# Kernel tuning notes

Measured on AMD Instinct MI355X. Metric: run time of the kernel, lower is better.

The kernel has to match this reference:

```python
import jax, jax.numpy as jnp
import numpy as np
import math

D_MODEL = 512
N_HEAD = 8
D_FF = 2048
B, S, S_ENC = 2, 2048, 2048
EPS = 1e-5


def _linear_params(key, d_in, d_out):
    kw, kb = jax.random.split(key)
    w = jax.random.normal(kw, (d_in, d_out), dtype=jnp.float32) * 0.02
    b = jax.random.normal(kb, (d_out,), dtype=jnp.float32) * 0.02
    return w, b


def setup_inputs() -> dict:
    key = jax.random.key(0)
    ks = jax.random.split(key, 16)
    dec = jax.random.normal(ks[0], (B, S, D_MODEL), dtype=jnp.float32)
    enc = jax.random.normal(ks[1], (B, S_ENC, D_MODEL), dtype=jnp.float32)
    src_mask = jnp.ones((B, 1, 1, S_ENC), dtype=jnp.int32)  # no padding
    tgt_mask = jnp.tril(jnp.ones((S, S), dtype=jnp.int32))[None, None]  # causal
    inp = {"dec": dec, "enc": enc, "src_mask": src_mask, "tgt_mask": tgt_mask}
    # self-attention projections
    for i, nm in enumerate(["sa_wq", "sa_wk", "sa_wv", "sa_wo"]):
        w, b = _linear_params(ks[2 + i], D_MODEL, D_MODEL)
        inp[nm], inp[nm.replace("w", "b")] = w, b
    # cross-attention projections
    for i, nm in enumerate(["ca_wq", "ca_wk", "ca_wv", "ca_wo"]):
        w, b = _linear_params(ks[6 + i], D_MODEL, D_MODEL)
        inp[nm], inp[nm.replace("w", "b")] = w, b
    # FFN
    inp["ffn_w1"], inp["ffn_b1"] = _linear_params(ks[10], D_MODEL, D_FF)
    inp["ffn_w2"], inp["ffn_b2"] = _linear_params(ks[11], D_FF, D_MODEL)
    # LayerNorms (gamma=1, beta=0 init as in torch)
    for i in (1, 2, 3):
        inp[f"ln{i}_g"] = jnp.ones((D_MODEL,), dtype=jnp.float32)
        inp[f"ln{i}_b"] = jnp.zeros((D_MODEL,), dtype=jnp.float32)
    return inp


def _layer_norm(x, g, b):
    mu = jnp.mean(x, axis=-1, keepdims=True)
    var = jnp.mean(jnp.square(x - mu), axis=-1, keepdims=True)
    return (x - mu) * jax.lax.rsqrt(var + EPS) * g + b


def _mha(xq, xkv, wq, bq, wk, bk, wv, bv, wo, bo, mask):
    Bq, Sq, D = xq.shape
    Sk = xkv.shape[1]
    d_k = D // N_HEAD
    def split(x, s):
        return x.reshape(x.shape[0], s, N_HEAD, d_k).transpose(0, 2, 1, 3)  # [B,H,S,dk]
    q = split(xq @ wq + bq, Sq)
    k = split(xkv @ wk + bk, Sk)
    v = split(xkv @ wv + bv, Sk)
    scores = jnp.einsum("bhqd,bhkd->bhqk", q, k) / math.sqrt(d_k)
    if mask is not None:
        scores = jnp.where(mask == 0, jnp.float32(-1e9), scores)
    attn = jax.nn.softmax(scores, axis=-1)
    out = jnp.einsum("bhqk,bhkd->bhqd", attn, v)
    out = out.transpose(0, 2, 1, 3).reshape(Bq, Sq, D)
    return out @ wo + bo


def reference(dec, enc, src_mask, tgt_mask,
              sa_wq, sa_bq, sa_wk, sa_bk, sa_wv, sa_bv, sa_wo, sa_bo,
              ca_wq, ca_bq, ca_wk, ca_bk, ca_wv, ca_bv, ca_wo, ca_bo,
              ffn_w1, ffn_b1, ffn_w2, ffn_b2,
              ln1_g, ln1_b, ln2_g, ln2_b, ln3_g, ln3_b):
    # dropout is identity in eval mode
    x = _mha(dec, dec, sa_wq, sa_bq, sa_wk, sa_bk, sa_wv, sa_bv, sa_wo, sa_bo, tgt_mask)
    x = _layer_norm(x + dec, ln1_g, ln1_b)
    _x = x
    x = _mha(x, enc, ca_wq, ca_bq, ca_wk, ca_bk, ca_wv, ca_bv, ca_wo, ca_bo, src_mask)
    x = _layer_norm(x + _x, ln2_g, ln2_b)
    _x = x
    x = jax.nn.relu(x @ ffn_w1 + ffn_b1) @ ffn_w2 + ffn_b2
    x = _layer_norm(x + _x, ln3_g, ln3_b)
    return x
```

## Files before the change

### kernel.cpp

```cpp
#include <hip/hip_runtime.h>


#define D_MODEL 512
#define NHEAD 8
#define DK 64
#define SEQ 2048
#define MTOK 4096
#define DFF 2048

typedef __attribute__((ext_vector_type(8))) short bf16x8;
typedef __attribute__((ext_vector_type(4))) float f32x4;

__device__ __forceinline__ unsigned short f2bf(float x) {
  unsigned u = __float_as_uint(x);
  u += 0x7FFF + ((u >> 16) & 1);
  return (unsigned short)(u >> 16);
}
__device__ __forceinline__ unsigned pack2(float a, float b) {
  return (unsigned)f2bf(a) | ((unsigned)f2bf(b) << 16);
}
__device__ __forceinline__ void load_lds16(const unsigned short* g, unsigned short* l) {
  __builtin_amdgcn_global_load_lds(
      (const __attribute__((address_space(1))) void*)g,
      (__attribute__((address_space(3))) void*)l, 16, 0, 0);
}

struct WDesc { const float* src; unsigned short* dst; int K; int N; };
struct WPack { WDesc d[10]; };

__global__ __launch_bounds__(256)
void wprep_kernel(WPack p) {
  const WDesc wd = p.d[blockIdx.y];
  const int ntx = wd.N >> 5;
  const int ntile = (wd.K >> 5) * ntx;
  if ((int)blockIdx.x >= ntile) return;
  const int n0 = (blockIdx.x % ntx) * 32;
  const int k0 = (blockIdx.x / ntx) * 32;
  __shared__ float T[32][33];
  const int tid = threadIdx.x;
  {
    const int r = tid >> 3, c4 = (tid & 7) * 4;
    float4 v = *(const float4*)(wd.src + (long)(k0 + r) * wd.N + n0 + c4);
    T[r][c4] = v.x; T[r][c4 + 1] = v.y; T[r][c4 + 2] = v.z; T[r][c4 + 3] = v.w;
  }
  __syncthreads();
  {
    const int n = tid >> 3, kq = (tid & 7) * 4;
    ushort4 o;
    o.x = f2bf(T[kq + 0][n]); o.y = f2bf(T[kq + 1][n]);
    o.z = f2bf(T[kq + 2][n]); o.w = f2bf(T[kq + 3][n]);
    *(ushort4*)(wd.dst + (long)(n0 + n) * wd.K + k0 + kq) = o;
  }
}

__global__ __launch_bounds__(256)
void cast_kernel(const float* __restrict__ s, unsigned short* __restrict__ d, int n8) {
  const int i = blockIdx.x * 256 + threadIdx.x;
  if (i >= n8) return;
  float4 a = *(const float4*)(s + (long)i * 8);
  float4 b = *(const float4*)(s + (long)i * 8 + 4);
  uint4 o;
  o.x = pack2(a.x, a.y); o.y = pack2(a.z, a.w);
  o.z = pack2(b.x, b.y); o.w = pack2(b.z, b.w);
  *(uint4*)(d + (long)i * 8) = o;
}

template<int MODE, int BM>
__global__ __launch_bounds__(256)
void gemm_bf16(const unsigned short* __restrict__ A, const unsigned short* __restrict__ Wt,
               const float* __restrict__ b0, const float* __restrict__ b1,
               const float* __restrict__ b2, const float* res,
               const float* __restrict__ lnm, const float* __restrict__ lnr,
               const float* __restrict__ lng, const float* __restrict__ lnbt,
               unsigned short* __restrict__ o0, unsigned short* __restrict__ o1,
               unsigned short* __restrict__ o2, float* of,
               int M, int N, int K, float scale0) {
  constexpr int MF = BM / 32;
  __shared__ unsigned short As[BM * 32];
  __shared__ unsigned short Bs[2048];
  const int tid = threadIdx.x;
  const int w = tid >> 6, lane = tid & 63, g = lane >> 4, li = lane & 15;
  const int m0 = blockIdx.x * BM, n0 = blockIdx.y * 64;
  const int wm = w >> 1, wn = w & 1;

  f32x4 acc[MF][2] = {};
  const int bkg = tid >> 6, bn = tid & 63;
  const unsigned short* Bp = Wt + (long)(n0 + bn) * K + bkg * 8;

  const unsigned short* Ap0;
  const unsigned short* Ap1 = nullptr;
  if constexpr (BM == 128) {
    Ap0 = A + (long)(m0 + (tid & 127)) * K + (tid >> 7) * 8;
    Ap1 = A + (long)(m0 + (tid & 127)) * K + ((tid >> 7) + 2) * 8;
  } else {
    Ap0 = A + (long)(m0 + (tid & 63)) * K + (tid >> 6) * 8;
  }

  for (int k0 = 0; k0 < K; k0 += 32) {
    __syncthreads();
    load_lds16(Ap0 + k0, &As[(w * 64) * 8]);
    if constexpr (BM == 128) load_lds16(Ap1 + k0, &As[(256 + w * 64) * 8]);
    load_lds16(Bp + k0, &Bs[(w * 64) * 8]);
    __syncthreads();
    bf16x8 af[MF], bfr[2];
#pragma unroll
    for (int mf = 0; mf < MF; mf++)
      af[mf] = *(const bf16x8*)&As[(g * BM + wm * (BM / 2) + mf * 16 + li) * 8];
#pragma unroll
    for (int nf = 0; nf < 2; nf++)
      bfr[nf] = *(const bf16x8*)&Bs[(g * 64 + wn * 32 + nf * 16 + li) * 8];
#pragma unroll
    for (int mf = 0; mf < MF; mf++)
#pragma unroll
      for (int nf = 0; nf < 2; nf++)
        acc[mf][nf] = __builtin_amdgcn_mfma_f32_16x16x32_bf16(af[mf], bfr[nf], acc[mf][nf], 0, 0, 0);
  }

#pragma unroll
  for (int nf = 0; nf < 2; nf++) {
    const int c = n0 + wn * 32 + nf * 16 + li;
    float bias, scl = 1.f;
    unsigned short* hdst = nullptr;
    float lngv = 0.f, lnbv = 0.f;
    if constexpr (MODE == 0) {
      const int which = c >> 9;
      bias = (which == 0 ? b0 : (which == 1 ? b1 : b2))[c & 511];
      if (which == 0) scl = scale0;
      hdst = which == 0 ? o0 : (which == 1 ? o1 : o2);
    } else {
      bias = b0[c];
      if constexpr (MODE == 3) { lngv = lng[c]; lnbv = lnbt[c]; }
    }
#pragma unroll
    for (int mf = 0; mf < MF; mf++) {
#pragma unroll
      for (int j = 0; j < 4; j++) {
        const int r = m0 + wm * (BM / 2) + mf * 16 + g * 4 + j;
        float v = acc[mf][nf][j] + bias;
        if constexpr (MODE == 0) {
          v *= scl;
          const int b = r >> 11, s = r & (SEQ - 1), h = (c >> 6) & 7, d = c & 63;
          hdst[(((long)(b * NHEAD + h)) * SEQ + s) * DK + d] = f2bf(v);
        } else if constexpr (MODE == 1) {
          v += res[(long)r * N + c];
          of[(long)r * N + c] = v;
        } else if constexpr (MODE == 2) {
          o0[(long)r * N + c] = f2bf(fmaxf(v, 0.f));
        } else {
          const float xr = res[(long)r * N + c];
          v += (xr - lnm[r]) * lnr[r] * lngv + lnbv;
          of[(long)r * N + c] = v;
        }
      }
    }
  }
}

template<bool CAUSAL>
__global__ __launch_bounds__(256)
void attn_bf16(const unsigned short* __restrict__ Qg, const unsigned short* __restrict__ Kg,
               const unsigned short* __restrict__ Vg, float* __restrict__ Opart,
               float* __restrict__ Mst, float* __restrict__ Lst) {
  __shared__ unsigned short SM[16384];
  unsigned short* const Qp = SM;
  unsigned short* const Kp = SM + 8192;
  unsigned short* const Vt = SM + 12288;
  const int tid = threadIdx.x;
  const int w = tid >> 6, lane = tid & 63, g = lane >> 4, li = lane & 15;
  const int qb = blockIdx.x, bh = blockIdx.y, ck = blockIdx.z;
  const int q0 = qb * 128;
  const long base = (long)bh * SEQ * DK;
  unsigned short* const Pl = SM + w * 2048;

#pragma unroll
  for (int i = 0; i < 4; i++) {
    const int idx = i * 256 + tid;
    const int dg = idx >> 7, q = idx & 127;
    load_lds16(Qg + base + (long)(q0 + q) * DK + dg * 8, &Qp[(i * 256 + w * 64) * 8]);
  }
  __syncthreads();
  bf16x8 bq[2][2];
#pragma unroll
  for (int qf = 0; qf < 2; qf++)
#pragma unroll
    for (int ks = 0; ks < 2; ks++)
      bq[qf][ks] = *(const bf16x8*)&Qp[((ks * 4 + g) * 128 + w * 32 + qf * 16 + li) * 8];

  f32x4 oacc[2][4] = {};
  float mrun[2] = {-1e30f, -1e30f};
  float denom[2] = {0.f, 0.f};

  const int vdg = tid >> 5;
  const int vs0 = (tid & 31) * 2;
  const int vsg = vs0 >> 3, vso = vs0 & 7;

  const int tbeg = CAUSAL ? ck : ck * 8;
  const int tend = CAUSAL ? (2 * qb + 2) : (ck * 8 + 8);
  const int tstep = CAUSAL ? 4 : 1;
  for (int t = tbeg; t < tend; t += tstep) {
    const int k0 = t * 64;
    __syncthreads();
#pragma unroll
    for (int i = 0; i < 2; i++) {
      const int idx = i * 256 + tid;
      const int dg = idx >> 6, kk = idx & 63;
      load_lds16(Kg + base + (long)(k0 + kk) * DK + dg * 8, &Kp[(i * 256 + w * 64) * 8]);
    }
    {
      const unsigned short* vsrc = Vg + base + (long)(k0 + vs0) * DK + vdg * 8;
      uint4 r0 = *(const uint4*)vsrc;
      uint4 r1 = *(const uint4*)(vsrc + DK);
      unsigned short u0[8], u1[8];
      *(uint4*)u0 = r0; *(uint4*)u1 = r1;
#pragma unroll
      for (int e = 0; e < 8; e++) {
        const int d = vdg * 8 + e;
        const int dsw = d ^ (vsg & 7);
        *(unsigned*)&Vt[(vsg * 64 + dsw) * 8 + vso] =
            (unsigned)u0[e] | ((unsigned)u1[e] << 16);
      }
    }
    __syncthreads();

    f32x4 sacc[4][2] = {};
#pragma unroll
    for (int ks = 0; ks < 2; ks++) {
#pragma unroll
      for (int kf = 0; kf < 4; kf++) {
        bf16x8 ka = *(const bf16x8*)&Kp[((ks * 4 + g) * 64 + kf * 16 + li) * 8];
#pragma unroll
        for (int qf = 0; qf < 2; qf++)
          sacc[kf][qf] = __builtin_amdgcn_mfma_f32_16x16x32_bf16(ka, bq[qf][ks], sacc[kf][qf], 0, 0, 0);
      }
    }
    if (CAUSAL && t >= 2 * qb) {
#pragma unroll
      for (int kf = 0; kf < 4; kf++)
#pragma unroll
        for (int qf = 0; qf < 2; qf++)
#pragma unroll
          for (int j = 0; j < 4; j++) {
            const int kg_ = k0 + kf * 16 + g * 4 + j;
            const int qg_ = q0 + w * 32 + qf * 16 + li;
            if (kg_ > qg_) sacc[kf][qf][j] = -1e30f;
          }
    }
    float corrv[2];
#pragma unroll
    for (int qf = 0; qf < 2; qf++) {
      float mx = -1e30f;
#pragma unroll
      for (int kf = 0; kf < 4; kf++)
#pragma unroll
        for (int j = 0; j < 4; j++) mx = fmaxf(mx, sacc[kf][qf][j]);
      mx = fmaxf(mx, __shfl_xor(mx, 16, 64));
      mx = fmaxf(mx, __shfl_xor(mx, 32, 64));
      const float mn = fmaxf(mrun[qf], mx);
      const float corr = exp2f(mrun[qf] - mn);
      mrun[qf] = mn;
      float ps = 0.f;
#pragma unroll
      for (int kf = 0; kf < 4; kf++)
#pragma unroll
        for (int j = 0; j < 4; j++) {
          const float p = exp2f(sacc[kf][qf][j] - mn);
          sacc[kf][qf][j] = p;
          ps += p;
        }
      ps += __shfl_xor(ps, 16, 64);
      ps += __shfl_xor(ps, 32, 64);
      denom[qf] = denom[qf] * corr + ps;
      corrv[qf] = corr;
    }
#pragma unroll
    for (int mf = 0; mf < 2; mf++)
#pragma unroll
      for (int j = 0; j < 4; j++) {
        const float cf = __shfl(corrv[mf], g * 4 + j, 64);
#pragma unroll
        for (int df = 0; df < 4; df++) oacc[mf][df][j] *= cf;
      }
#pragma unroll
    for (int kf = 0; kf < 4; kf++)
#pragma unroll
      for (int qf = 0; qf < 2; qf++) {
        uint2 pv;
        pv.x = pack2(sacc[kf][qf][0], sacc[kf][qf][1]);
        pv.y = pack2(sacc[kf][qf][2], sacc[kf][qf][3]);
        *(uint2*)&Pl[((kf * 2 + (g >> 1)) * 32 + qf * 16 + li) * 8 + (g & 1) * 4] = pv;
      }
#pragma unroll
    for (int ks2 = 0; ks2 < 2; ks2++) {
      const int sg = ks2 * 4 + g;
#pragma unroll
      for (int mf = 0; mf < 2; mf++) {
        bf16x8 pa = *(const bf16x8*)&Pl[(sg * 32 + mf * 16 + li) * 8];
#pragma unroll
        for (int df = 0; df < 4; df++) {
          bf16x8 vb = *(const bf16x8*)&Vt[(sg * 64 + ((df * 16 + li) ^ (sg & 7))) * 8];
          oacc[mf][df] = __builtin_amdgcn_mfma_f32_16x16x32_bf16(pa, vb, oacc[mf][df], 0, 0, 0);
        }
      }
    }
  }

  const long pbase = (long)(ck * 16 + bh) * SEQ;
  if (g == 0) {
#pragma unroll
    for (int qf = 0; qf < 2; qf++) {
      const int q = q0 + w * 32 + qf * 16 + li;
      Mst[pbase + q] = mrun[qf];
      Lst[pbase + q] = denom[qf];
    }
  }
#pragma unroll
  for (int mf = 0; mf < 2; mf++)
#pragma unroll
    for (int j = 0; j < 4; j++) {
      const int q = q0 + w * 32 + mf * 16 + g * 4 + j;
      float* op = Opart + (pbase + q) * 64;
#pragma unroll
      for (int df = 0; df < 4; df++) op[df * 16 + li] = oacc[mf][df][j];
    }
}

__global__ __launch_bounds__(256)
void combine_kernel(const float* __restrict__ Opart, const float* __restrict__ Mst,
                    const float* __restrict__ Lst, unsigned short* __restrict__ AOb) {
  const int row = blockIdx.x * 4 + (threadIdx.x >> 6);
  const int lane = threadIdx.x & 63;
  const int bh = row >> 11, q = row & (SEQ - 1);
  float m[4], l[4], mstar = -1e30f;
#pragma unroll
  for (int c = 0; c < 4; c++) {
    m[c] = Mst[((long)c * 16 + bh) * SEQ + q];
    l[c] = Lst[((long)c * 16 + bh) * SEQ + q];
    mstar = fmaxf(mstar, m[c]);
  }
  float den = 0.f, o = 0.f;
#pragma unroll
  for (int c = 0; c < 4; c++) {
    const float wgt = exp2f(m[c] - mstar);
    den += wgt * l[c];
    o += wgt * Opart[(((long)c * 16 + bh) * SEQ + q) * 64 + lane];
  }
  const int b = bh >> 3, h = bh & 7;
  AOb[((long)(b * SEQ + q)) * D_MODEL + h * DK + lane] = f2bf(o / den);
}

template<int V>
__global__ __launch_bounds__(256)
void ln_kernel(const float* __restrict__ x, const float* __restrict__ gam,
               const float* __restrict__ bet, float* __restrict__ outf,
               unsigned short* __restrict__ outb, float* __restrict__ mu_s,
               float* __restrict__ rs_s) {
  const int row = blockIdx.x * 4 + (threadIdx.x >> 6);
  const int lane = threadIdx.x & 63;
  const float* xr = x + (long)row * D_MODEL;
  float4 v0 = *(const float4*)&xr[lane * 8];
  float4 v1 = *(const float4*)&xr[lane * 8 + 4];
  float xv[8] = {v0.x, v0.y, v0.z, v0.w, v1.x, v1.y, v1.z, v1.w};
  float s = 0.f, s2 = 0.f;
#pragma unroll
  for (int i = 0; i < 8; i++) { s += xv[i]; s2 = fmaf(xv[i], xv[i], s2); }
#pragma unroll
  for (int off = 32; off > 0; off >>= 1) {
    s += __shfl_xor(s, off, 64);
    s2 += __shfl_xor(s2, off, 64);
  }
  const float mu = s * (1.f / D_MODEL);
  const float var = fmaxf(s2 * (1.f / D_MODEL) - mu * mu, 0.f);
  const float rstd = rsqrtf(var + 1e-5f);
  float y[8];
#pragma unroll
  for (int i = 0; i < 8; i++) {
    const int c = lane * 8 + i;
    y[i] = (xv[i] - mu) * rstd * gam[c] + bet[c];
  }
  if constexpr (V == 0) {
    uint4 o;
    o.x = pack2(y[0], y[1]); o.y = pack2(y[2], y[3]);
    o.z = pack2(y[4], y[5]); o.w = pack2(y[6], y[7]);
    *(uint4*)(outb + (long)row * D_MODEL + lane * 8) = o;
    if (lane == 0) { mu_s[row] = mu; rs_s[row] = rstd; }
  } else {
    float* orow = outf + (long)row * D_MODEL + lane * 8;
    *(float4*)orow = make_float4(y[0], y[1], y[2], y[3]);
    *(float4*)(orow + 4) = make_float4(y[4], y[5], y[6], y[7]);
  }
}

extern "C" void kernel_launch(void* const* d_in, const int* in_sizes, int n_in,
                              void* d_out, int out_size, void* d_ws, size_t ws_size,
                              hipStream_t stream) {
  const float* dec = (const float*)d_in[0];
  const float* enc = (const float*)d_in[1];
  const float* sa_wq = (const float*)d_in[4];
  const float* sa_bq = (const float*)d_in[5];
  const float* sa_wk = (const float*)d_in[6];
  const float* sa_bk = (const float*)d_in[7];
  const float* sa_wv = (const float*)d_in[8];
  const float* sa_bv = (const float*)d_in[9];
  const float* sa_wo = (const float*)d_in[10];
  const float* sa_bo = (const float*)d_in[11];
  const float* ca_wq = (const float*)d_in[12];
  const float* ca_bq = (const float*)d_in[13];
  const float* ca_wk = (const float*)d_in[14];
  const float* ca_bk = (const float*)d_in[15];
  const float* ca_wv = (const float*)d_in[16];
  const float* ca_bv = (const float*)d_in[17];
  const float* ca_wo = (const float*)d_in[18];
  const float* ca_bo = (const float*)d_in[19];
  const float* ffn_w1 = (const float*)d_in[20];
  const float* ffn_b1 = (const float*)d_in[21];
  const float* ffn_w2 = (const float*)d_in[22];
  const float* ffn_b2 = (const float*)d_in[23];
  const float* ln1_g = (const float*)d_in[24];
  const float* ln1_b = (const float*)d_in[25];
  const float* ln2_g = (const float*)d_in[26];
  const float* ln2_b = (const float*)d_in[27];
  const float* ln3_g = (const float*)d_in[28];
  const float* ln3_b = (const float*)d_in[29];

  char* wsb = (char*)d_ws;
  unsigned short* dec_bf = (unsigned short*)wsb;
  float* Opart = (float*)wsb;
  float* Mst = (float*)(wsb + 33554432);
  float* Lst = (float*)(wsb + 34078720);
  unsigned short* MIDb = (unsigned short*)wsb;
  size_t off = 34603008;
  unsigned short* qkv_t = (unsigned short*)(wsb + off); off += 1572864;
  unsigned short* wo_t  = (unsigned short*)(wsb + off); off += 524288;
  unsigned short* cq_t  = (unsigned short*)(wsb + off); off += 524288;
  unsigned short* ckv_t = (unsigned short*)(wsb + off); off += 1048576;
  unsigned short* co_t  = (unsigned short*)(wsb + off); off += 524288;
  unsigned short* f1_t  = (unsigned short*)(wsb + off); off += 2097152;
  unsigned short* f2_t  = (unsigned short*)(wsb + off); off += 2097152;
  unsigned short* enc_bf = (unsigned short*)(wsb + off); off += 4194304;
  unsigned short* Qb  = (unsigned short*)(wsb + off); off += 4194304;
  unsigned short* Kb  = (unsigned short*)(wsb + off); off += 4194304;
  unsigned short* Vb  = (unsigned short*)(wsb + off); off += 4194304;
  unsigned short* AOb = (unsigned short*)(wsb + off); off += 4194304;
  unsigned short* X1b = (unsigned short*)(wsb + off); off += 4194304;
  unsigned short* X2b = (unsigned short*)(wsb + off); off += 4194304;
  float* R   = (float*)(wsb + off); off += 8388608;
  float* mu1 = (float*)(wsb + off); off += 16384;
  float* rs1 = (float*)(wsb + off); off += 16384;
  float* mu2 = (float*)(wsb + off); off += 16384;
  float* rs2 = (float*)(wsb + off); off += 16384;

  dim3 blk(256);
  const float QS = 0.125f * 1.44269504f;

  WPack wp;
  wp.d[0] = {sa_wq, qkv_t, 512, 512};
  wp.d[1] = {sa_wk, qkv_t + 262144, 512, 512};
  wp.d[2] = {sa_wv, qkv_t + 524288, 512, 512};
  wp.d[3] = {sa_wo, wo_t, 512, 512};
  wp.d[4] = {ca_wq, cq_t, 512, 512};
  wp.d[5] = {ca_wk, ckv_t, 512, 512};
  wp.d[6] = {ca_wv, ckv_t + 262144, 512, 512};
  wp.d[7] = {ca_wo, co_t, 512, 512};
  wp.d[8] = {ffn_w1, f1_t, 512, 2048};
  wp.d[9] = {ffn_w2, f2_t, 2048, 512};
  wprep_kernel<<<dim3(1024, 10), blk, 0, stream>>>(wp);
  cast_kernel<<<1024, blk, 0, stream>>>(dec, dec_bf, 262144);
  cast_kernel<<<1024, blk, 0, stream>>>(enc, enc_bf, 262144);

  gemm_bf16<0, 128><<<dim3(32, 24), blk, 0, stream>>>(dec_bf, qkv_t, sa_bq, sa_bk, sa_bv,
      nullptr, nullptr, nullptr, nullptr, nullptr, Qb, Kb, Vb, nullptr, MTOK, 1536, 512, QS);
  attn_bf16<true><<<dim3(16, 16, 4), blk, 0, stream>>>(Qb, Kb, Vb, Opart, Mst, Lst);
  combine_kernel<<<8192, blk, 0, stream>>>(Opart, Mst, Lst, AOb);
  gemm_bf16<1, 64><<<dim3(64, 8), blk, 0, stream>>>(AOb, wo_t, sa_bo, nullptr, nullptr,
      dec, nullptr, nullptr, nullptr, nullptr, nullptr, nullptr, nullptr, R, MTOK, 512, 512, 1.f);
  ln_kernel<0><<<1024, blk, 0, stream>>>(R, ln1_g, ln1_b, nullptr, X1b, mu1, rs1);

  gemm_bf16<0, 64><<<dim3(64, 8), blk, 0, stream>>>(X1b, cq_t, ca_bq, nullptr, nullptr,
      nullptr, nullptr, nullptr, nullptr, nullptr, Qb, nullptr, nullptr, nullptr, MTOK, 512, 512, QS);
  gemm_bf16<0, 128><<<dim3(32, 16), blk, 0, stream>>>(enc_bf, ckv_t, ca_bk, ca_bv, nullptr,
      nullptr, nullptr, nullptr, nullptr, nullptr, Kb, Vb, nullptr, nullptr, MTOK, 1024, 512, 1.f);
  attn_bf16<false><<<dim3(16, 16, 4), blk, 0, stream>>>(Qb, Kb, Vb, Opart, Mst, Lst);
  combine_kernel<<<8192, blk, 0, stream>>>(Opart, Mst, Lst, AOb);
  gemm_bf16<3, 64><<<dim3(64, 8), blk, 0, stream>>>(AOb, co_t, ca_bo, nullptr, nullptr,
      R, mu1, rs1, ln1_g, ln1_b, nullptr, nullptr, nullptr, R, MTOK, 512, 512, 1.f);
  ln_kernel<0><<<1024, blk, 0, stream>>>(R, ln2_g, ln2_b, nullptr, X2b, mu2, rs2);

  gemm_bf16<2, 128><<<dim3(32, 32), blk, 0, stream>>>(X2b, f1_t, ffn_b1, nullptr, nullptr,
      nullptr, nullptr, nullptr, nullptr, nullptr, MIDb, nullptr, nullptr, nullptr, MTOK, 2048, 512, 1.f);
  gemm_bf16<3, 64><<<dim3(64, 8), blk, 0, stream>>>(MIDb, f2_t, ffn_b2, nullptr, nullptr,
      R, mu2, rs2, ln2_g, ln2_b, nullptr, nullptr, nullptr, R, MTOK, 512, 2048, 1.f);
  ln_kernel<1><<<1024, blk, 0, stream>>>(R, ln3_g, ln3_b, (float*)d_out, nullptr, nullptr, nullptr);
}
```

Before: 435.0 us.

## Generalize GEMM tile width, add lazy softmax rescale and fast exp/bf16 pack

The GEMM kernel gains a BN template parameter so all launches use 128x128 or 128x64 tiles, which increases reuse per block and reduces the block count. The attention softmax now skips the running-max update and the output rescale unless some row's max grows by more than 8 (in log2 units), leaving the lazy rescaling decision uniform across the wave. exp2f is replaced with the hardware exp2 builtin, and bf16 packing uses the v_cvt_pk_bf16_f32 instruction. Larger tiles cut occupancy and leave fewer blocks for the 512x512 GEMMs, which can hurt load balance across the 256 CUs.

```diff
diff --git a/kernel.cpp b/kernel.cpp
--- a/kernel.cpp
+++ b/kernel.cpp
@@ -11,6 +11,12 @@
 typedef __attribute__((ext_vector_type(8))) short bf16x8;
 typedef __attribute__((ext_vector_type(4))) float f32x4;
 
+#if __has_builtin(__builtin_amdgcn_exp2f)
+#define EXP2(x) __builtin_amdgcn_exp2f(x)
+#else
+#define EXP2(x) exp2f(x)
+#endif
+
 __device__ __forceinline__ unsigned short f2bf(float x) {
   unsigned u = __float_as_uint(x);
   u += 0x7FFF + ((u >> 16) & 1);
@@ -18,6 +24,11 @@
 }
 __device__ __forceinline__ unsigned pack2(float a, float b) {
   return (unsigned)f2bf(a) | ((unsigned)f2bf(b) << 16);
+}
+__device__ __forceinline__ unsigned cvtpk(float lo, float hi) {
+  unsigned r;
+  asm("v_cvt_pk_bf16_f32 %0, %1, %2" : "=v"(r) : "v"(lo), "v"(hi));
+  return r;
 }
 __device__ __forceinline__ void load_lds16(const unsigned short* g, unsigned short* l) {
   __builtin_amdgcn_global_load_lds(
@@ -65,7 +76,7 @@
   *(uint4*)(d + (long)i * 8) = o;
 }
 
-template<int MODE, int BM>
+template<int MODE, int BM, int BN>
 __global__ __launch_bounds__(256)
 void gemm_bf16(const unsigned short* __restrict__ A, const unsigned short* __restrict__ Wt,
                const float* __restrict__ b0, const float* __restrict__ b1,
@@ -75,50 +86,53 @@
                unsigned short* __restrict__ o0, unsigned short* __restrict__ o1,
                unsigned short* __restrict__ o2, float* of,
                int M, int N, int K, float scale0) {
-  constexpr int MF = BM / 32;
+  constexpr int MF = BM / 32, NF = BN / 32;
+  constexpr int AI = BM / 64, BI = BN / 64;
   __shared__ unsigned short As[BM * 32];
-  __shared__ unsigned short Bs[2048];
+  __shared__ unsigned short Bs[BN * 32];
   const int tid = threadIdx.x;
   const int w = tid >> 6, lane = tid & 63, g = lane >> 4, li = lane & 15;
-  const int m0 = blockIdx.x * BM, n0 = blockIdx.y * 64;
+  const int m0 = blockIdx.x * BM, n0 = blockIdx.y * BN;
   const int wm = w >> 1, wn = w & 1;
 
-  f32x4 acc[MF][2] = {};
-  const int bkg = tid >> 6, bn = tid & 63;
-  const unsigned short* Bp = Wt + (long)(n0 + bn) * K + bkg * 8;
-
-  const unsigned short* Ap0;
-  const unsigned short* Ap1 = nullptr;
-  if constexpr (BM == 128) {
-    Ap0 = A + (long)(m0 + (tid & 127)) * K + (tid >> 7) * 8;
-    Ap1 = A + (long)(m0 + (tid & 127)) * K + ((tid >> 7) + 2) * 8;
-  } else {
-    Ap0 = A + (long)(m0 + (tid & 63)) * K + (tid >> 6) * 8;
+  f32x4 acc[MF][NF] = {};
+  const unsigned short* Ap[AI];
+  const unsigned short* Bp[BI];
+#pragma unroll
+  for (int i = 0; i < AI; i++) {
+    const int idx = i * 256 + tid;
+    Ap[i] = A + (long)(m0 + (idx % BM)) * K + (idx / BM) * 8;
+  }
+#pragma unroll
+  for (int i = 0; i < BI; i++) {
+    const int idx = i * 256 + tid;
+    Bp[i] = Wt + (long)(n0 + (idx % BN)) * K + (idx / BN) * 8;
   }
 
   for (int k0 = 0; k0 < K; k0 += 32) {
     __syncthreads();
-    load_lds16(Ap0 + k0, &As[(w * 64) * 8]);
-    if constexpr (BM == 128) load_lds16(Ap1 + k0, &As[(256 + w * 64) * 8]);
-    load_lds16(Bp + k0, &Bs[(w * 64) * 8]);
+#pragma unroll
+    for (int i = 0; i < AI; i++) load_lds16(Ap[i] + k0, &As[(i * 256 + w * 64) * 8]);
+#pragma unroll
+    for (int i = 0; i < BI; i++) load_lds16(Bp[i] + k0, &Bs[(i * 256 + w * 64) * 8]);
     __syncthreads();
-    bf16x8 af[MF], bfr[2];
+    bf16x8 af[MF], bfr[NF];
 #pragma unroll
     for (int mf = 0; mf < MF; mf++)
       af[mf] = *(const bf16x8*)&As[(g * BM + wm * (BM / 2) + mf * 16 + li) * 8];
 #pragma unroll
-    for (int nf = 0; nf < 2; nf++)
-      bfr[nf] = *(const bf16x8*)&Bs[(g * 64 + wn * 32 + nf * 16 + li) * 8];
+    for (int nf = 0; nf < NF; nf++)
+      bfr[nf] = *(const bf16x8*)&Bs[(g * BN + wn * (BN / 2) + nf * 16 + li) * 8];
 #pragma unroll
     for (int mf = 0; mf < MF; mf++)
 #pragma unroll
-      for (int nf = 0; nf < 2; nf++)
+      for (int nf = 0; nf < NF; nf++)
         acc[mf][nf] = __builtin_amdgcn_mfma_f32_16x16x32_bf16(af[mf], bfr[nf], acc[mf][nf], 0, 0, 0);
   }
 
 #pragma unroll
-  for (int nf = 0; nf < 2; nf++) {
-    const int c = n0 + wn * 32 + nf * 16 + li;
+  for (int nf = 0; nf < NF; nf++) {
+    const int c = n0 + wn * (BN / 2) + nf * 16 + li;
     float bias, scl = 1.f;
     unsigned short* hdst = nullptr;
     float lngv = 0.f, lnbv = 0.f;
@@ -245,48 +259,60 @@
             if (kg_ > qg_) sacc[kf][qf][j] = -1e30f;
           }
     }
-    float corrv[2];
+    float mx[2];
 #pragma unroll
     for (int qf = 0; qf < 2; qf++) {
-      float mx = -1e30f;
+      float a = fmaxf(fmaxf(sacc[0][qf][0], sacc[0][qf][1]), fmaxf(sacc[0][qf][2], sacc[0][qf][3]));
+      float b = fmaxf(fmaxf(sacc[1][qf][0], sacc[1][qf][1]), fmaxf(sacc[1][qf][2], sacc[1][qf][3]));
+      float c = fmaxf(fmaxf(sacc[2][qf][0], sacc[2][qf][1]), fmaxf(sacc[2][qf][2], sacc[2][qf][3]));
+      float d = fmaxf(fmaxf(sacc[3][qf][0], sacc[3][qf][1]), fmaxf(sacc[3][qf][2], sacc[3][qf][3]));
+      float m_ = fmaxf(fmaxf(a, b), fmaxf(c, d));
+      m_ = fmaxf(m_, __shfl_xor(m_, 16, 64));
+      m_ = fmaxf(m_, __shfl_xor(m_, 32, 64));
+      mx[qf] = m_;
+    }
+    const int full = !__all((mx[0] - mrun[0] <= 8.f) && (mx[1] - mrun[1] <= 8.f));
+    float corrv[2] = {1.f, 1.f};
+    if (full) {
+#pragma unroll
+      for (int qf = 0; qf < 2; qf++) {
+        const float mn = fmaxf(mrun[qf], mx[qf]);
+        corrv[qf] = EXP2(mrun[qf] - mn);
+        mrun[qf] = mn;
+      }
+    }
+#pragma unroll
+    for (int qf = 0; qf < 2; qf++) {
+      float ps = 0.f;
 #pragma unroll
       for (int kf = 0; kf < 4; kf++)
 #pragma unroll
-        for (int j = 0; j < 4; j++) mx = fmaxf(mx, sacc[kf][qf][j]);
-      mx = fmaxf(mx, __shfl_xor(mx, 16, 64));
-      mx = fmaxf(mx, __shfl_xor(mx, 32, 64));
-      const float mn = fmaxf(mrun[qf], mx);
-      const float corr = exp2f(mrun[qf] - mn);
-      mrun[qf] = mn;
-      float ps = 0.f;
-#pragma unroll
-      for (int kf = 0; kf < 4; kf++)
-#pragma unroll
         for (int j = 0; j < 4; j++) {
-          const float p = exp2f(sacc[kf][qf][j] - mn);
+          const float p = EXP2(sacc[kf][qf][j] - mrun[qf]);
           sacc[kf][qf][j] = p;
           ps += p;
         }
       ps += __shfl_xor(ps, 16, 64);
       ps += __shfl_xor(ps, 32, 64);
-      denom[qf] = denom[qf] * corr + ps;
-      corrv[qf] = corr;
-    }
-#pragma unroll
-    for (int mf = 0; mf < 2; mf++)
-#pragma unroll
-      for (int j = 0; j < 4; j++) {
-        const float cf = __shfl(corrv[mf], g * 4 + j, 64);
-#pragma unroll
-        for (int df = 0; df < 4; df++) oacc[mf][df][j] *= cf;
-      }
+      denom[qf] = denom[qf] * corrv[qf] + ps;
+    }
+    if (full) {
+#pragma unroll
+      for (int mf = 0; mf < 2; mf++)
+#pragma unroll
+        for (int j = 0; j < 4; j++) {
+          const float cf = __shfl(corrv[mf], g * 4 + j, 64);
+#pragma unroll
+          for (int df = 0; df < 4; df++) oacc[mf][df][j] *= cf;
+        }
+    }
 #pragma unroll
     for (int kf = 0; kf < 4; kf++)
 #pragma unroll
       for (int qf = 0; qf < 2; qf++) {
         uint2 pv;
-        pv.x = pack2(sacc[kf][qf][0], sacc[kf][qf][1]);
-        pv.y = pack2(sacc[kf][qf][2], sacc[kf][qf][3]);
+        pv.x = cvtpk(sacc[kf][qf][0], sacc[kf][qf][1]);
+        pv.y = cvtpk(sacc[kf][qf][2], sacc[kf][qf][3]);
         *(uint2*)&Pl[((kf * 2 + (g >> 1)) * 32 + qf * 16 + li) * 8 + (g & 1) * 4] = pv;
       }
 #pragma unroll
@@ -340,7 +366,7 @@
   float den = 0.f, o = 0.f;
 #pragma unroll
   for (int c = 0; c < 4; c++) {
-    const float wgt = exp2f(m[c] - mstar);
+    const float wgt = EXP2(m[c] - mstar);
     den += wgt * l[c];
     o += wgt * Opart[(((long)c * 16 + bh) * SEQ + q) * 64 + lane];
   }
@@ -467,27 +493,27 @@
   cast_kernel<<<1024, blk, 0, stream>>>(dec, dec_bf, 262144);
   cast_kernel<<<1024, blk, 0, stream>>>(enc, enc_bf, 262144);
 
-  gemm_bf16<0, 128><<<dim3(32, 24), blk, 0, stream>>>(dec_bf, qkv_t, sa_bq, sa_bk, sa_bv,
+  gemm_bf16<0, 128, 128><<<dim3(32, 12), blk, 0, stream>>>(dec_bf, qkv_t, sa_bq, sa_bk, sa_bv,
       nullptr, nullptr, nullptr, nullptr, nullptr, Qb, Kb, Vb, nullptr, MTOK, 1536, 512, QS);
   attn_bf16<true><<<dim3(16, 16, 4), blk, 0, stream>>>(Qb, Kb, Vb, Opart, Mst, Lst);
   combine_kernel<<<8192, blk, 0, stream>>>(Opart, Mst, Lst, AOb);
-  gemm_bf16<1, 64><<<dim3(64, 8), blk, 0, stream>>>(AOb, wo_t, sa_bo, nullptr, nullptr,
+  gemm_bf16<1, 128, 64><<<dim3(32, 8), blk, 0, stream>>>(AOb, wo_t, sa_bo, nullptr, nullptr,
       dec, nullptr, nullptr, nullptr, nullptr, nullptr, nullptr, nullptr, R, MTOK, 512, 512, 1.f);
   ln_kernel<0><<<1024, blk, 0, stream>>>(R, ln1_g, ln1_b, nullptr, X1b, mu1, rs1);
 
-  gemm_bf16<0, 64><<<dim3(64, 8), blk, 0, stream>>>(X1b, cq_t, ca_bq, nullptr, nullptr,
+  gemm_bf16<0, 128, 64><<<dim3(32, 8), blk, 0, stream>>>(X1b, cq_t, ca_bq, nullptr, nullptr,
       nullptr, nullptr, nullptr, nullptr, nullptr, Qb, nullptr, nullptr, nullptr, MTOK, 512, 512, QS);
-  gemm_bf16<0, 128><<<dim3(32, 16), blk, 0, stream>>>(enc_bf, ckv_t, ca_bk, ca_bv, nullptr,
+  gemm_bf16<0, 128, 128><<<dim3(32, 8), blk, 0, stream>>>(enc_bf, ckv_t, ca_bk, ca_bv, nullptr,
       nullptr, nullptr, nullptr, nullptr, nullptr, Kb, Vb, nullptr, nullptr, MTOK, 1024, 512, 1.f);
   attn_bf16<false><<<dim3(16, 16, 4), blk, 0, stream>>>(Qb, Kb, Vb, Opart, Mst, Lst);
   combine_kernel<<<8192, blk, 0, stream>>>(Opart, Mst, Lst, AOb);
-  gemm_bf16<3, 64><<<dim3(64, 8), blk, 0, stream>>>(AOb, co_t, ca_bo, nullptr, nullptr,
+  gemm_bf16<3, 128, 64><<<dim3(32, 8), blk, 0, stream>>>(AOb, co_t, ca_bo, nullptr, nullptr,
       R, mu1, rs1, ln1_g, ln1_b, nullptr, nullptr, nullptr, R, MTOK, 512, 512, 1.f);
   ln_kernel<0><<<1024, blk, 0, stream>>>(R, ln2_g, ln2_b, nullptr, X2b, mu2, rs2);
 
-  gemm_bf16<2, 128><<<dim3(32, 32), blk, 0, stream>>>(X2b, f1_t, ffn_b1, nullptr, nullptr,
+  gemm_bf16<2, 128, 128><<<dim3(32, 16), blk, 0, stream>>>(X2b, f1_t, ffn_b1, nullptr, nullptr,
       nullptr, nullptr, nullptr, nullptr, nullptr, MIDb, nullptr, nullptr, nullptr, MTOK, 2048, 512, 1.f);
-  gemm_bf16<3, 64><<<dim3(64, 8), blk, 0, stream>>>(MIDb, f2_t, ffn_b2, nullptr, nullptr,
+  gemm_bf16<3, 128, 64><<<dim3(32, 8), blk, 0, stream>>>(MIDb, f2_t, ffn_b2, nullptr, nullptr,
       R, mu2, rs2, ln2_g, ln2_b, nullptr, nullptr, nullptr, R, MTOK, 512, 2048, 1.f);
   ln_kernel<1><<<1024, blk, 0, stream>>>(R, ln3_g, ln3_b, (float*)d_out, nullptr, nullptr, nullptr);
 }
```

Measured after the change: 435.5 us. About the same (+0.1%).
